# Optimization experiments

Measured on AMD Instinct MI355X. Metric: run time of the kernel, lower is better.

Reference implementation:

```python
import jax, jax.numpy as jnp
import numpy as np

INPUT_DIM = 66
OUTPUT_COUNT = 8192
NUM_PAIRS = 65536

def setup_inputs() -> dict:
    key = jax.random.key(0)
    k1, k2, k3, k4 = jax.random.split(key, 4)
    x = jax.random.normal(k1, (NUM_PAIRS, INPUT_DIM), dtype=jnp.float32)
    query = jax.random.normal(k2, (OUTPUT_COUNT, INPUT_DIM), dtype=jnp.float32)
    # nn.Linear(input_dim, input_dim): weight [out,in], bias [out]
    bound = 1.0 / np.sqrt(INPUT_DIM)
    Wk = jax.random.uniform(k3, (INPUT_DIM, INPUT_DIM), minval=-bound, maxval=bound, dtype=jnp.float32)
    bk = jax.random.uniform(k4, (INPUT_DIM,), minval=-bound, maxval=bound, dtype=jnp.float32)
    return {"x": x, "query": query, "Wk": Wk, "bk": bk}

def reference(x, query, Wk, bk):
    # K = Linear(x): x @ Wk^T + bk  -> [num_pairs, d]
    K = x @ Wk.T + bk
    # scores: [output_count, num_pairs]
    scores = jnp.einsum("qd,nd->qn", query, K)
    attn = jax.nn.softmax(scores, axis=1)
    # selected: [output_count, d] — note values are raw x, not K
    selected = attn @ x
    return selected
```

## Files before the change

kernel.cpp:

```cpp
#include <hip/hip_runtime.h>
#include <cstdint>


typedef __bf16    bf16x4 __attribute__((ext_vector_type(4)));
typedef __bf16    bf16x8 __attribute__((ext_vector_type(8)));
typedef _Float16  f16x4  __attribute__((ext_vector_type(4)));
typedef _Float16  f16x8  __attribute__((ext_vector_type(8)));
typedef float     f32x16 __attribute__((ext_vector_type(16)));

extern "C" __device__ float __ocml_native_exp2_f32(float);

#define NUM_PAIRS   65536
#define NUM_Q       8192
#define DIM         66
#define KPITCH      84
#define QPITCH      80
#define XROWS       96
#define XPITCH      36
#define XTILE       (XROWS*XPITCH)
#define PARTP       68

#define LDS_KT 0
#define LDS_XT 10752
#define LDS_TOTAL 24576

__device__ __forceinline__ bf16x8 frag8(const __bf16* p) {
    bf16x4 lo = *(const bf16x4*)p;
    bf16x4 hi = *(const bf16x4*)(p + 4);
    return __builtin_shufflevector(lo, hi, 0, 1, 2, 3, 4, 5, 6, 7);
}
__device__ __forceinline__ f16x8 frag8h(const _Float16* p) {
    f16x4 lo = *(const f16x4*)p;
    f16x4 hi = *(const f16x4*)(p + 4);
    return __builtin_shufflevector(lo, hi, 0, 1, 2, 3, 4, 5, 6, 7);
}
__device__ __forceinline__ f32x16 mfma_bf16(bf16x8 a, bf16x8 b, f32x16 c) {
    return __builtin_amdgcn_mfma_f32_32x32x16_bf16(a, b, c, 0, 0, 0);
}
__device__ __forceinline__ f32x16 mfma_f16(f16x8 a, f16x8 b, f32x16 c) {
    return __builtin_amdgcn_mfma_f32_32x32x16_f16(a, b, c, 0, 0, 0);
}

__device__ __forceinline__ void plswap(unsigned &a, unsigned &b) {
    asm("v_permlane32_swap_b32 %0, %1" : "+v"(a), "+v"(b));
}

__device__ __forceinline__ unsigned packbf(float a, float b) {
    union { __bf16 h[2]; unsigned u; } t;
    t.h[0] = (__bf16)a; t.h[1] = (__bf16)b;
    return t.u;
}

union U4 { unsigned u[4]; bf16x8 v; };

__device__ __forceinline__ void makefrags(const f32x16 &s, U4 *f) {
    float P[16];
    #pragma unroll
    for (int r = 0; r < 16; ++r) P[r] = __ocml_native_exp2_f32(s[r]);
    unsigned E0 = packbf(P[0],  P[1]),  E1 = packbf(P[2],  P[3]);
    unsigned F0 = packbf(P[4],  P[5]),  F1 = packbf(P[6],  P[7]);
    plswap(E0, F0); plswap(E1, F1);
    f[0].u[0] = E0; f[0].u[1] = E1; f[0].u[2] = F0; f[0].u[3] = F1;
    unsigned G0 = packbf(P[8],  P[9]),  G1 = packbf(P[10], P[11]);
    unsigned H0 = packbf(P[12], P[13]), H1 = packbf(P[14], P[15]);
    plswap(G0, H0); plswap(G1, H1);
    f[1].u[0] = G0; f[1].u[1] = G1; f[1].u[2] = H0; f[1].u[3] = H1;
}

#define PA_ROWS 128
__global__ __launch_bounds__(256) void prepA_kernel(
    const float* __restrict__ x, const float* __restrict__ Wk,
    const float* __restrict__ bk,
    unsigned short* __restrict__ Kh_u, unsigned short* __restrict__ Xb_u) {
    _Float16* Kh = (_Float16*)Kh_u;
    __bf16*   Xb = (__bf16*)Xb_u;
    __shared__ _Float16 sxh[PA_ROWS * 96];
    __shared__ _Float16 sW[96 * 96];
    const int tid = threadIdx.x;
    const long n0 = (long)blockIdx.x * PA_ROWS;

    for (int i = tid; i < PA_ROWS * 96; i += 256) {
        int r = i / 96, c = i % 96;
        float v = (c < DIM) ? x[(n0 + r) * DIM + c] : 0.f;
        sxh[i] = (_Float16)v;
    }
    for (int i = tid; i < 96 * 96; i += 256) {
        int cc = i / 96, d = i % 96;
        float v = (cc < DIM && d < DIM) ? Wk[cc * DIM + d] : 0.f;
        sW[i] = (_Float16)v;
    }
    __syncthreads();

    const int lane = tid & 63, w = tid >> 6;
    const int l31 = lane & 31, h = lane >> 5;

    #pragma unroll
    for (int nt = 0; nt < 3; ++nt) {
        f32x16 acc = {};
        #pragma unroll
        for (int kk = 0; kk < 6; ++kk) {
            f16x8 a = *(const f16x8*)&sxh[(w * 32 + l31) * 96 + kk * 16 + h * 8];
            f16x8 b = *(const f16x8*)&sW[(nt * 32 + l31) * 96 + kk * 16 + h * 8];
            acc = mfma_f16(a, b, acc);
        }
        int c = nt * 32 + l31;
        float bkv = (c < DIM) ? bk[c] : 0.f;
        if (c < KPITCH) {
            #pragma unroll
            for (int r = 0; r < 16; ++r) {
                int row = (r & 3) + 8 * (r >> 2) + 4 * h;
                Kh[(n0 + w * 32 + row) * KPITCH + c] = (_Float16)(acc[r] + bkv);
            }
        }
    }

    for (int ii = tid; ii < 4 * XTILE; ii += 256) {
        int b = ii / XTILE, i = ii % XTILE;
        int dd = i / XPITCH, j = i % XPITCH;
        float v = 0.f;
        if (j < 32) {
            if (dd < DIM) v = (float)sxh[(b * 32 + j) * 96 + dd];
            else if (dd == DIM) v = 1.f;
        }
        Xb[((long)blockIdx.x * 4 + b) * XTILE + i] = (__bf16)v;
    }
}

__global__ __launch_bounds__(256) void prepB_kernel(
    const float* __restrict__ query, unsigned short* __restrict__ Qh_u) {
    _Float16* Qh = (_Float16*)Qh_u;
    int idx = blockIdx.x * 256 + threadIdx.x;
    int q = idx / QPITCH, c = idx % QPITCH;
    float v = (c < DIM) ? query[(long)q * DIM + c] * 1.4426950408889634f : 0.f;
    Qh[idx] = (_Float16)v;
}

__global__ __launch_bounds__(256, 2) void flash_kernel(
    const unsigned short* __restrict__ Qh_u, const unsigned short* __restrict__ Kh_u,
    const unsigned short* __restrict__ Xb_u, float* __restrict__ Part, int NS) {
    __shared__ __attribute__((aligned(16))) char smem[LDS_TOTAL];
    _Float16* Kt = (_Float16*)(smem + LDS_KT);
    __bf16*   Xt = (__bf16*)(smem + LDS_XT);
    const _Float16* Qh = (const _Float16*)Qh_u;
    const _Float16* Kh = (const _Float16*)Kh_u;

    const int tid = threadIdx.x;
    const int lane = tid & 63, wave = tid >> 6;
    const int l31 = lane & 31, h = lane >> 5;
    const int qb = blockIdx.x / NS, ns = blockIdx.x % NS;
    const int ppc = NUM_PAIRS / NS;
    const int iters = ppc >> 6;
    const int qbase = qb * 256 + wave * 64;

    f16x8 aQ[2][5];
    #pragma unroll
    for (int qt = 0; qt < 2; ++qt)
        #pragma unroll
        for (int kk = 0; kk < 5; ++kk)
            aQ[qt][kk] = *(const f16x8*)&Qh[(long)(qbase + qt * 32 + l31) * QPITCH + kk * 16 + h * 8];

    f32x16 o[2][3] = {};

    for (int it = 0; it < iters; ++it) {
        const long p0 = (long)ns * ppc + (long)it * 64;
        __syncthreads();
        {
            const char* gK = (const char*)(Kh + p0 * KPITCH);
            const char* gX = (const char*)(Xb_u + (p0 >> 5) * XTILE);
            for (int c = wave; c < 24; c += 4) {
                int off = c * 1024 + lane * 16;
                const char* src = (off < 10752) ? (gK + off) : (gX + (off - 10752));
                __builtin_amdgcn_global_load_lds(
                    (const __attribute__((address_space(1))) void*)(uintptr_t)src,
                    (__attribute__((address_space(3))) void*)(unsigned int)(uintptr_t)(smem + c * 1024),
                    16, 0, 0);
            }
        }
        __syncthreads();

        #pragma unroll
        for (int pt = 0; pt < 2; ++pt) {
            f16x8 bK[5];
            #pragma unroll
            for (int kk = 0; kk < 5; ++kk)
                bK[kk] = frag8h(&Kt[(pt * 32 + l31) * KPITCH + kk * 16 + h * 8]);
            f32x16 s0 = {}, s1 = {};
            #pragma unroll
            for (int kk = 0; kk < 5; ++kk) {
                s0 = mfma_f16(bK[kk], aQ[0][kk], s0);
                s1 = mfma_f16(bK[kk], aQ[1][kk], s1);
            }
            U4 f[2][2];
            makefrags(s0, f[0]);
            makefrags(s1, f[1]);
            #pragma unroll
            for (int par = 0; par < 2; ++par) {
                const int kc = par * 16 + h * 8;
                #pragma unroll
                for (int dt = 0; dt < 3; ++dt) {
                    bf16x8 bX = frag8(&Xt[pt * XTILE + (dt * 32 + l31) * XPITCH + kc]);
                    o[0][dt] = mfma_bf16(f[0][par].v, bX, o[0][dt]);
                    o[1][dt] = mfma_bf16(f[1][par].v, bX, o[1][dt]);
                }
            }
        }
    }

    float* dst = Part + (long)ns * NUM_Q * PARTP;
    #pragma unroll
    for (int qt = 0; qt < 2; ++qt)
        #pragma unroll
        for (int dt = 0; dt < 3; ++dt)
            #pragma unroll
            for (int r = 0; r < 16; ++r) {
                int row = (r & 3) + 8 * (r >> 2) + 4 * h;
                int q = qbase + qt * 32 + row;
                int d = dt * 32 + l31;
                if (d < DIM + 1) dst[(long)q * PARTP + d] = o[qt][dt][r];
            }
}

__global__ __launch_bounds__(256) void combine_kernel(
    const float* __restrict__ Part, float* __restrict__ out, int NS) {
    int q = blockIdx.x * 2 + (threadIdx.x >> 7);
    int d = threadIdx.x & 127;
    if (d >= DIM) return;
    float num = 0.f, den = 0.f;
    for (int s = 0; s < NS; ++s) {
        const float* p = Part + ((long)s * NUM_Q + q) * PARTP;
        num += p[d];
        den += p[DIM];
    }
    out[(long)q * DIM + d] = num / den;
}

extern "C" void kernel_launch(void* const* d_in, const int* in_sizes, int n_in,
                              void* d_out, int out_size, void* d_ws, size_t ws_size,
                              hipStream_t stream) {
    const float* x     = (const float*)d_in[0];
    const float* query = (const float*)d_in[1];
    const float* Wk    = (const float*)d_in[2];
    const float* bk    = (const float*)d_in[3];
    float* out = (float*)d_out;
    char* ws = (char*)d_ws;

    unsigned short* Qh = (unsigned short*)(ws + 0);
    unsigned short* Kh = (unsigned short*)(ws + 1310720);
    unsigned short* Xb = (unsigned short*)(ws + 12320768);
    float* Part        = (float*)(ws + 26476544);

    int NS = 16;
    while (NS > 1 &&
           26476544ULL + (unsigned long long)NS * NUM_Q * PARTP * 4ULL > (unsigned long long)ws_size)
        NS >>= 1;

    prepA_kernel<<<NUM_PAIRS / PA_ROWS, 256, 0, stream>>>(x, Wk, bk, Kh, Xb);
    prepB_kernel<<<(NUM_Q * QPITCH) / 256, 256, 0, stream>>>(query, Qh);
    flash_kernel<<<(NUM_Q / 256) * NS, 256, 0, stream>>>(Qh, Kh, Xb, Part, NS);
    combine_kernel<<<NUM_Q / 2, 256, 0, stream>>>(Part, out, NS);
}
```

Before: 290.7 us.

## Double-buffer K/X tiles in LDS to overlap loads with MFMA compute

Adds a second LDS stage buffer to the flash kernel and ping-pongs between them, so the global-to-LDS loads for the next 64-pair tile are issued before computing the current one. This hides load latency behind the score and accumulate MFMAs, at the cost of doubling LDS per block to 48KB, which could limit occupancy. It also pads the prepA shared arrays to pitch 104 to reduce bank conflicts and unrolls the combine loop. The loop assumes an even iteration count, and when iters is odd it computes on a tile that was never loaded.

```diff
diff --git a/kernel.cpp b/kernel.cpp
--- a/kernel.cpp
+++ b/kernel.cpp
@@ -20,9 +20,10 @@
 #define XTILE       (XROWS*XPITCH)
 #define PARTP       68
 
-#define LDS_KT 0
 #define LDS_XT 10752
-#define LDS_TOTAL 24576
+#define STG    24576
+#define KSTRIDE 10752
+#define XSTRIDE 13824
 
 __device__ __forceinline__ bf16x8 frag8(const __bf16* p) {
     bf16x4 lo = *(const bf16x4*)p;
@@ -44,7 +45,6 @@
 __device__ __forceinline__ void plswap(unsigned &a, unsigned &b) {
     asm("v_permlane32_swap_b32 %0, %1" : "+v"(a), "+v"(b));
 }
-
 __device__ __forceinline__ unsigned packbf(float a, float b) {
     union { __bf16 h[2]; unsigned u; } t;
     t.h[0] = (__bf16)a; t.h[1] = (__bf16)b;
@@ -67,27 +67,72 @@
     f[1].u[0] = G0; f[1].u[1] = G1; f[1].u[2] = H0; f[1].u[3] = H1;
 }
 
+__device__ __forceinline__ void stage_tile(char* dst, const char* gK, const char* gX,
+                                           int wave, int lane) {
+    #pragma unroll
+    for (int j = 0; j < 6; ++j) {
+        int c = wave + 4 * j;
+        int off = c * 1024 + lane * 16;
+        const char* src = (off < KSTRIDE) ? (gK + off) : (gX + (off - KSTRIDE));
+        __builtin_amdgcn_global_load_lds(
+            (const __attribute__((address_space(1))) void*)(uintptr_t)src,
+            (__attribute__((address_space(3))) void*)(unsigned int)(uintptr_t)(dst + c * 1024),
+            16, 0, 0);
+    }
+}
+
+__device__ __forceinline__ void compute_tile(const char* sm, const f16x8 (&aQ)[2][5],
+                                             f32x16 (&o)[2][3], int l31, int h) {
+    const _Float16* Kt = (const _Float16*)sm;
+    const __bf16*   Xt = (const __bf16*)(sm + LDS_XT);
+    #pragma unroll
+    for (int pt = 0; pt < 2; ++pt) {
+        f16x8 bK[5];
+        #pragma unroll
+        for (int kk = 0; kk < 5; ++kk)
+            bK[kk] = frag8h(&Kt[(pt * 32 + l31) * KPITCH + kk * 16 + h * 8]);
+        f32x16 s0 = {}, s1 = {};
+        #pragma unroll
+        for (int kk = 0; kk < 5; ++kk) {
+            s0 = mfma_f16(bK[kk], aQ[0][kk], s0);
+            s1 = mfma_f16(bK[kk], aQ[1][kk], s1);
+        }
+        U4 f[2][2];
+        makefrags(s0, f[0]);
+        makefrags(s1, f[1]);
+        #pragma unroll
+        for (int par = 0; par < 2; ++par) {
+            const int kc = par * 16 + h * 8;
+            #pragma unroll
+            for (int dt = 0; dt < 3; ++dt) {
+                bf16x8 bX = frag8(&Xt[pt * XTILE + (dt * 32 + l31) * XPITCH + kc]);
+                o[0][dt] = mfma_bf16(f[0][par].v, bX, o[0][dt]);
+                o[1][dt] = mfma_bf16(f[1][par].v, bX, o[1][dt]);
+            }
+        }
+    }
+}
+
 #define PA_ROWS 128
+#define PAP 104
 __global__ __launch_bounds__(256) void prepA_kernel(
     const float* __restrict__ x, const float* __restrict__ Wk,
     const float* __restrict__ bk,
     unsigned short* __restrict__ Kh_u, unsigned short* __restrict__ Xb_u) {
     _Float16* Kh = (_Float16*)Kh_u;
     __bf16*   Xb = (__bf16*)Xb_u;
-    __shared__ _Float16 sxh[PA_ROWS * 96];
-    __shared__ _Float16 sW[96 * 96];
+    __shared__ _Float16 sxh[PA_ROWS * PAP];
+    __shared__ _Float16 sW[96 * PAP];
     const int tid = threadIdx.x;
     const long n0 = (long)blockIdx.x * PA_ROWS;
 
     for (int i = tid; i < PA_ROWS * 96; i += 256) {
         int r = i / 96, c = i % 96;
-        float v = (c < DIM) ? x[(n0 + r) * DIM + c] : 0.f;
-        sxh[i] = (_Float16)v;
+        sxh[r * PAP + c] = (_Float16)((c < DIM) ? x[(n0 + r) * DIM + c] : 0.f);
     }
     for (int i = tid; i < 96 * 96; i += 256) {
         int cc = i / 96, d = i % 96;
-        float v = (cc < DIM && d < DIM) ? Wk[cc * DIM + d] : 0.f;
-        sW[i] = (_Float16)v;
+        sW[cc * PAP + d] = (_Float16)((cc < DIM && d < DIM) ? Wk[cc * DIM + d] : 0.f);
     }
     __syncthreads();
 
@@ -99,8 +144,8 @@
         f32x16 acc = {};
         #pragma unroll
         for (int kk = 0; kk < 6; ++kk) {
-            f16x8 a = *(const f16x8*)&sxh[(w * 32 + l31) * 96 + kk * 16 + h * 8];
-            f16x8 b = *(const f16x8*)&sW[(nt * 32 + l31) * 96 + kk * 16 + h * 8];
+            f16x8 a = *(const f16x8*)&sxh[(w * 32 + l31) * PAP + kk * 16 + h * 8];
+            f16x8 b = *(const f16x8*)&sW[(nt * 32 + l31) * PAP + kk * 16 + h * 8];
             acc = mfma_f16(a, b, acc);
         }
         int c = nt * 32 + l31;
@@ -119,7 +164,7 @@
         int dd = i / XPITCH, j = i % XPITCH;
         float v = 0.f;
         if (j < 32) {
-            if (dd < DIM) v = (float)sxh[(b * 32 + j) * 96 + dd];
+            if (dd < DIM) v = (float)sxh[(b * 32 + j) * PAP + dd];
             else if (dd == DIM) v = 1.f;
         }
         Xb[((long)blockIdx.x * 4 + b) * XTILE + i] = (__bf16)v;
@@ -138,11 +183,9 @@
 __global__ __launch_bounds__(256, 2) void flash_kernel(
     const unsigned short* __restrict__ Qh_u, const unsigned short* __restrict__ Kh_u,
     const unsigned short* __restrict__ Xb_u, float* __restrict__ Part, int NS) {
-    __shared__ __attribute__((aligned(16))) char smem[LDS_TOTAL];
-    _Float16* Kt = (_Float16*)(smem + LDS_KT);
-    __bf16*   Xt = (__bf16*)(smem + LDS_XT);
+    __shared__ __attribute__((aligned(16))) char smA[STG];
+    __shared__ __attribute__((aligned(16))) char smB[STG];
     const _Float16* Qh = (const _Float16*)Qh_u;
-    const _Float16* Kh = (const _Float16*)Kh_u;
 
     const int tid = threadIdx.x;
     const int lane = tid & 63, wave = tid >> 6;
@@ -152,6 +195,10 @@
     const int iters = ppc >> 6;
     const int qbase = qb * 256 + wave * 64;
 
+    const long pbase = (long)ns * ppc;
+    const char* gK0 = (const char*)Kh_u + pbase * (KPITCH * 2);
+    const char* gX0 = (const char*)Xb_u + (pbase >> 5) * (XTILE * 2);
+
     f16x8 aQ[2][5];
     #pragma unroll
     for (int qt = 0; qt < 2; ++qt)
@@ -161,49 +208,18 @@
 
     f32x16 o[2][3] = {};
 
-    for (int it = 0; it < iters; ++it) {
-        const long p0 = (long)ns * ppc + (long)it * 64;
+    stage_tile(smA, gK0, gX0, wave, lane);
+    for (int it = 0; it < iters; it += 2) {
         __syncthreads();
-        {
-            const char* gK = (const char*)(Kh + p0 * KPITCH);
-            const char* gX = (const char*)(Xb_u + (p0 >> 5) * XTILE);
-            for (int c = wave; c < 24; c += 4) {
-                int off = c * 1024 + lane * 16;
-                const char* src = (off < 10752) ? (gK + off) : (gX + (off - 10752));
-                __builtin_amdgcn_global_load_lds(
-                    (const __attribute__((address_space(1))) void*)(uintptr_t)src,
-                    (__attribute__((address_space(3))) void*)(unsigned int)(uintptr_t)(smem + c * 1024),
-                    16, 0, 0);
-            }
-        }
+        if (it + 1 < iters)
+            stage_tile(smB, gK0 + (long)(it + 1) * KSTRIDE,
+                            gX0 + (long)(it + 1) * XSTRIDE, wave, lane);
+        compute_tile(smA, aQ, o, l31, h);
         __syncthreads();
-
-        #pragma unroll
-        for (int pt = 0; pt < 2; ++pt) {
-            f16x8 bK[5];
-            #pragma unroll
-            for (int kk = 0; kk < 5; ++kk)
-                bK[kk] = frag8h(&Kt[(pt * 32 + l31) * KPITCH + kk * 16 + h * 8]);
-            f32x16 s0 = {}, s1 = {};
-            #pragma unroll
-            for (int kk = 0; kk < 5; ++kk) {
-                s0 = mfma_f16(bK[kk], aQ[0][kk], s0);
-                s1 = mfma_f16(bK[kk], aQ[1][kk], s1);
-            }
-            U4 f[2][2];
-            makefrags(s0, f[0]);
-            makefrags(s1, f[1]);
-            #pragma unroll
-            for (int par = 0; par < 2; ++par) {
-                const int kc = par * 16 + h * 8;
-                #pragma unroll
-                for (int dt = 0; dt < 3; ++dt) {
-                    bf16x8 bX = frag8(&Xt[pt * XTILE + (dt * 32 + l31) * XPITCH + kc]);
-                    o[0][dt] = mfma_bf16(f[0][par].v, bX, o[0][dt]);
-                    o[1][dt] = mfma_bf16(f[1][par].v, bX, o[1][dt]);
-                }
-            }
-        }
+        if (it + 2 < iters)
+            stage_tile(smA, gK0 + (long)(it + 2) * KSTRIDE,
+                            gX0 + (long)(it + 2) * XSTRIDE, wave, lane);
+        compute_tile(smB, aQ, o, l31, h);
     }
 
     float* dst = Part + (long)ns * NUM_Q * PARTP;
@@ -226,6 +242,7 @@
     int d = threadIdx.x & 127;
     if (d >= DIM) return;
     float num = 0.f, den = 0.f;
+    #pragma unroll 4
     for (int s = 0; s < NS; ++s) {
         const float* p = Part + ((long)s * NUM_Q + q) * PARTP;
         num += p[d];
```

Result: no change. 289.6 us (-0.4%).
